# Kernel tuning notes

Hardware: AMD Instinct MI355X
Metric: run time of the kernel (lower is better)

The kernel has to match this reference:

```python
import jax, jax.numpy as jnp
import numpy as np

H = 16          # num_heads
KVH = 4         # num_kv_heads
HD = 128        # head_dim = dim // num_heads
BASE = 10000.0  # rope_base
EPS = 1.1920928955078125e-07  # torch F.rms_norm default eps = finfo(fp32).eps


def rotate_half(x):
    h = x.shape[-1] // 2
    return jnp.concatenate([-x[..., h:], x[..., :h]], axis=-1)


def rms_norm(x):
    return x * jax.lax.rsqrt(jnp.mean(x * x, axis=-1, keepdims=True) + EPS)


def setup_inputs() -> dict:
    key = jax.random.key(0)
    ks = jax.random.split(key, 5)
    D = H * HD
    KVD = KVH * HD
    s = 0.02
    x = jax.random.normal(ks[0], (4, 2048, D), jnp.float32)
    Wq = jax.random.normal(ks[1], (D, D), jnp.float32) * s
    Wk = jax.random.normal(ks[2], (KVD, D), jnp.float32) * s
    Wv = jax.random.normal(ks[3], (KVD, D), jnp.float32) * s
    Wproj = jax.random.normal(ks[4], (D, D), jnp.float32) * s
    q_gain = jnp.full((H,), 1.0, jnp.float32)
    return {"x": x, "Wq": Wq, "Wk": Wk, "Wv": Wv, "Wproj": Wproj, "q_gain": q_gain}


def reference(x, Wq, Wk, Wv, Wproj, q_gain):
    B, T, D = x.shape
    # QKV projections (bias-free), reshape to [B, heads, T, head_dim]
    q = (x @ Wq.T).reshape(B, T, H, HD).transpose(0, 2, 1, 3)
    k = (x @ Wk.T).reshape(B, T, KVH, HD).transpose(0, 2, 1, 3)
    v = (x @ Wv.T).reshape(B, T, KVH, HD).transpose(0, 2, 1, 3)
    # QK RMSNorm (no learned weight)
    q = rms_norm(q)
    k = rms_norm(k)
    # Rotary embedding tables [T, HD]
    t = jnp.arange(T, dtype=jnp.float32)
    inv_freq = 1.0 / (BASE ** (jnp.arange(0, HD, 2, dtype=jnp.float32) / HD))
    freqs = jnp.outer(t, inv_freq)
    emb = jnp.concatenate([freqs, freqs], axis=-1)
    cos, sin = jnp.cos(emb), jnp.sin(emb)
    # RoPE + per-head gain on q
    q = (q * cos + rotate_half(q) * sin) * q_gain[None, :, None, None]
    k = k * cos + rotate_half(k) * sin
    # GQA: repeat_interleave kv heads to match q heads
    groups = H // KVH
    k = jnp.repeat(k, groups, axis=1)
    v = jnp.repeat(v, groups, axis=1)
    # Causal scaled dot-product attention
    scores = jnp.einsum('bhqd,bhkd->bhqk', q, k) / np.float32(np.sqrt(HD))
    mask = jnp.tril(jnp.ones((T, T), dtype=bool))
    scores = jnp.where(mask, scores, -jnp.inf)
    attn = jax.nn.softmax(scores, axis=-1)
    y = jnp.einsum('bhqk,bhkd->bhqd', attn, v)
    y = y.transpose(0, 2, 1, 3).reshape(B, T, D)
    return y @ Wproj.T
```

## Files before the change

kernel.cpp:

```cpp
#include <hip/hip_runtime.h>
#include <math.h>


typedef float f32x4 __attribute__((ext_vector_type(4)));
typedef __bf16 bf16x8 __attribute__((ext_vector_type(8)));
typedef __bf16 bf16x4 __attribute__((ext_vector_type(4)));
typedef __bf16 bf16x2 __attribute__((ext_vector_type(2)));

__device__ __forceinline__ void load_lds16(const __bf16* g, __bf16* l) {
    __builtin_amdgcn_global_load_lds(
        (const __attribute__((address_space(1))) void*)g,
        (__attribute__((address_space(3))) void*)l, 16, 0, 0);
}

__device__ __forceinline__ unsigned pack_bf16(float lo, float hi) {
    union { bf16x2 v; unsigned u; } c;
    c.v = bf16x2{(__bf16)lo, (__bf16)hi};
    return c.u;
}

__global__ __launch_bounds__(256) void cvt_all(
    const float* __restrict__ x,  const float* __restrict__ Wq,
    const float* __restrict__ Wk, const float* __restrict__ Wv,
    const float* __restrict__ Wp, __bf16* __restrict__ dst)
{
    long long i = ((long long)blockIdx.x * 256 + threadIdx.x) * 4;
    if (i >= 27262976LL) return;
    const float* src;
    long long off;
    if (i < 16777216LL)      { src = x;  off = i; }
    else if (i < 20971520LL) { src = Wq; off = i - 16777216LL; }
    else if (i < 22020096LL) { src = Wk; off = i - 20971520LL; }
    else if (i < 23068672LL) { src = Wv; off = i - 22020096LL; }
    else                     { src = Wp; off = i - 23068672LL; }
    float4 v = *(const float4*)(src + off);
    bf16x4 o = {(__bf16)v.x, (__bf16)v.y, (__bf16)v.z, (__bf16)v.w};
    *(bf16x4*)(dst + i) = o;
}

template <typename OutT>
__global__ __launch_bounds__(512, 2) void gemm8ph(
    const __bf16* __restrict__ A, const __bf16* __restrict__ W,
    OutT* __restrict__ C, int M, int N, int K)
{
    const int bm = blockIdx.x, bn = blockIdx.y;
    const int tid = threadIdx.x;
    const int lane = tid & 63, wave = tid >> 6;
    const int quad = lane >> 4, l16 = lane & 15;
    const int wm2 = wave >> 2;
    const int wn4 = wave & 3;

    __shared__ __bf16 As[2][256 * 64];
    __shared__ __bf16 Bs[2][256 * 64];

    f32x4 acc[8][4] = {};

    const int sr = tid >> 3;
    const int sc = tid & 7;
    const int scs = sc ^ (((sr >> 2) & 1) << 1);
    const __bf16* Ag = A + (size_t)(bm * 256 + sr) * K + scs * 8;
    const __bf16* Wg = W + (size_t)(bn * 256 + sr) * K + scs * 8;
    const int dst = sr * 64 + sc * 8;

    auto stA = [&](int t, int r) {
        load_lds16(Ag + (size_t)(r * 64) * K + t * 64,
                   &As[t & 1][r * 4096 + dst]);
    };
    auto stB = [&](int t, int r) {
        load_lds16(Wg + (size_t)(r * 64) * K + t * 64,
                   &Bs[t & 1][r * 4096 + dst]);
    };

    const int NT = K / 64;
    const int swzr = ((l16 >> 2) & 1) << 1;

#pragma unroll
    for (int r = 0; r < 4; ++r) { stA(0, r); stB(0, r); }
#pragma unroll
    for (int r = 0; r < 4; ++r) { stA(1, r); stB(1, r); }
    asm volatile("s_waitcnt vmcnt(8)" ::: "memory");
    __builtin_amdgcn_s_barrier();

    bf16x8 bfr[4][2];

    for (int i = 0; i < NT / 2; ++i) {
        const int t0 = 2 * i;
#pragma unroll
        for (int tt = 0; tt < 2; ++tt) {
            const __bf16* Ab = &As[tt][0];
            const __bf16* Bb = &Bs[tt][0];
#pragma unroll
            for (int qq = 0; qq < 4; ++qq) {
                bf16x8 af[2][2];
#pragma unroll
                for (int j = 0; j < 2; ++j)
#pragma unroll
                    for (int ks = 0; ks < 2; ++ks)
                        af[j][ks] = *(const bf16x8*)(
                            Ab + (wm2 * 128 + (qq * 2 + j) * 16 + l16) * 64 +
                            ((ks * 4 + quad) ^ swzr) * 8);
                if (qq == 0) {
#pragma unroll
                    for (int ni = 0; ni < 4; ++ni)
#pragma unroll
                        for (int ks = 0; ks < 2; ++ks)
                            bfr[ni][ks] = *(const bf16x8*)(
                                Bb + (wn4 * 64 + ni * 16 + l16) * 64 +
                                ((ks * 4 + quad) ^ swzr) * 8);
                }

                const int p = tt * 4 + qq;
                switch (p) {
                    case 0: if (i > 0) { stA(t0 + 1, 1); stA(t0 + 1, 3); } break;
                    case 1: if (t0 + 2 < NT) { stB(t0 + 2, 0); stB(t0 + 2, 1); } break;
                    case 2: if (t0 + 2 < NT) { stA(t0 + 2, 0); stA(t0 + 2, 2); } break;
                    case 3: if (t0 + 2 < NT) { stB(t0 + 2, 2); stB(t0 + 2, 3); } break;
                    case 4: if (t0 + 2 < NT) { stA(t0 + 2, 1); stA(t0 + 2, 3); } break;
                    case 5: if (t0 + 3 < NT) { stB(t0 + 3, 0); stB(t0 + 3, 1); } break;
                    case 6: if (t0 + 3 < NT) { stA(t0 + 3, 0); stA(t0 + 3, 2); } break;
                    case 7: if (t0 + 3 < NT) { stB(t0 + 3, 2); stB(t0 + 3, 3); } break;
                }
                if (qq == 3)
                    asm volatile("s_waitcnt vmcnt(6)" ::: "memory");

                __builtin_amdgcn_s_barrier();
                asm volatile("s_waitcnt lgkmcnt(0)" ::: "memory");
                __builtin_amdgcn_sched_barrier(0);
                __builtin_amdgcn_s_setprio(1);
#pragma unroll
                for (int j = 0; j < 2; ++j)
#pragma unroll
                    for (int ni = 0; ni < 4; ++ni)
#pragma unroll
                        for (int ks = 0; ks < 2; ++ks)
                            acc[qq * 2 + j][ni] =
                                __builtin_amdgcn_mfma_f32_16x16x32_bf16(
                                    af[j][ks], bfr[ni][ks],
                                    acc[qq * 2 + j][ni], 0, 0, 0);
                __builtin_amdgcn_s_setprio(0);
                __builtin_amdgcn_s_barrier();
            }
        }
    }

#pragma unroll
    for (int mi = 0; mi < 8; ++mi) {
#pragma unroll
        for (int r = 0; r < 4; ++r) {
            int row = bm * 256 + wm2 * 128 + mi * 16 + quad * 4 + r;
            OutT* Cp = C + (size_t)row * N + bn * 256 + wn4 * 64 + l16;
#pragma unroll
            for (int ni = 0; ni < 4; ++ni)
                Cp[ni * 16] = (OutT)acc[mi][ni][r];
        }
    }
}

template <int NI, typename OutT>
__global__ __launch_bounds__(512, 2) void gemm4buf(
    const __bf16* __restrict__ A, const __bf16* __restrict__ W,
    OutT* __restrict__ C, int M, int N, int K)
{
    constexpr int BN = 64 * NI;
    constexpr int WN = 16 * NI;
    const int bm = blockIdx.x, bn = blockIdx.y;
    const int tid = threadIdx.x;
    const int lane = tid & 63;
    const int wave = tid >> 6;
    const int quad = lane >> 4, l16 = lane & 15;
    const int wm2 = wave >> 2;
    const int wn4 = wave & 3;

    __shared__ __bf16 As[4][256 * 32];
    __shared__ __bf16 Bs[4][BN * 32];

    f32x4 acc[8][NI] = {};

    const int sr = tid >> 2;
    const int sc = tid & 3;
    const int scs = sc ^ (sr & 3) ^ ((sr >> 2) & 3);
    const int swzq = quad ^ (l16 & 3) ^ ((l16 >> 2) & 3);

    const __bf16* Ag = A + (size_t)(bm * 256 + sr) * K + scs * 8;
    const __bf16* Wg = W + (size_t)(bn * BN + sr) * K + scs * 8;
    const int dA = sr * 32 + sc * 8;

    auto stageB = [&](int t) {
        const int k0 = t * 32, buf = t & 3;
        load_lds16(Wg + k0, &Bs[buf][dA]);
        if constexpr (NI == 4)
            load_lds16(Wg + (size_t)128 * K + k0, &Bs[buf][128 * 32 + dA]);
    };
    auto stageA = [&](int t) {
        const int k0 = t * 32, buf = t & 3;
        load_lds16(Ag + k0, &As[buf][dA]);
        load_lds16(Ag + (size_t)128 * K + k0, &As[buf][128 * 32 + dA]);
    };
    auto waitAhead = [&](int ahead) {
        if constexpr (NI == 4) {
            if (ahead >= 2)      asm volatile("s_waitcnt vmcnt(8)" ::: "memory");
            else if (ahead == 1) asm volatile("s_waitcnt vmcnt(4)" ::: "memory");
            else                 asm volatile("s_waitcnt vmcnt(0)" ::: "memory");
        } else {
            if (ahead >= 2)      asm volatile("s_waitcnt vmcnt(6)" ::: "memory");
            else if (ahead == 1) asm volatile("s_waitcnt vmcnt(3)" ::: "memory");
            else                 asm volatile("s_waitcnt vmcnt(0)" ::: "memory");
        }
    };

    const int NT = K / 32;

    stageB(0); stageA(0);
    stageB(1); stageA(1);
    stageB(2); stageA(2);
    waitAhead(2);
    asm volatile("" ::: "memory");
    __builtin_amdgcn_s_barrier();
    asm volatile("" ::: "memory");

    for (int t = 0; t < NT; ++t) {
        const __bf16* Ab = &As[t & 3][0];
        const __bf16* Bb = &Bs[t & 3][0];
        const bool pf = (t + 3 < NT);

        bf16x8 bfr[NI];
#pragma unroll
        for (int ni = 0; ni < NI; ++ni)
            bfr[ni] = *(const bf16x8*)(
                Bb + (wn4 * WN + ni * 16 + l16) * 32 + swzq * 8);
        if (pf) stageB(t + 3);

        bf16x8 af[8];
#pragma unroll
        for (int mi = 0; mi < 8; ++mi)
            af[mi] = *(const bf16x8*)(
                Ab + (wm2 * 128 + mi * 16 + l16) * 32 + swzq * 8);
        if (pf) stageA(t + 3);

        __builtin_amdgcn_s_setprio(1);
#pragma unroll
        for (int mi = 0; mi < 8; ++mi)
#pragma unroll
            for (int ni = 0; ni < NI; ++ni)
                acc[mi][ni] = __builtin_amdgcn_mfma_f32_16x16x32_bf16(
                    af[mi], bfr[ni], acc[mi][ni], 0, 0, 0);
        __builtin_amdgcn_s_setprio(0);

        if (t + 1 < NT) {
            const int hi = (t + 3 < NT - 1) ? (t + 3) : (NT - 1);
            waitAhead(hi - (t + 1));
            asm volatile("" ::: "memory");
            __builtin_amdgcn_s_barrier();
            asm volatile("" ::: "memory");
        }
    }

#pragma unroll
    for (int mi = 0; mi < 8; ++mi) {
#pragma unroll
        for (int r = 0; r < 4; ++r) {
            int row = bm * 256 + wm2 * 128 + mi * 16 + quad * 4 + r;
            OutT* Cp = C + (size_t)row * N + bn * BN + wn4 * WN + l16;
#pragma unroll
            for (int ni = 0; ni < NI; ++ni)
                Cp[ni * 16] = (OutT)acc[mi][ni][r];
        }
    }
}

__global__ __launch_bounds__(256) void k_norm_rope(__bf16* __restrict__ kv)
{
    const int row = blockIdx.x * 4 + (threadIdx.x >> 6);
    const int lane = threadIdx.x & 63;
    const int bt = row >> 2, kvh = row & 3;
    __bf16* base = kv + (size_t)bt * 1024 + kvh * 128;
    const int t = bt & 2047;

    float x0 = (float)base[lane];
    float x1 = (float)base[lane + 64];

    float ss = x0 * x0 + x1 * x1;
#pragma unroll
    for (int off = 32; off; off >>= 1) ss += __shfl_xor(ss, off);
    float inv = rsqrtf(ss * (1.0f / 128.0f) + 1.1920928955078125e-07f);
    x0 *= inv; x1 *= inv;

    float freq = exp2f(-(float)lane * 0.20762050593046013f);
    float s, c;
    __sincosf((float)t * freq, &s, &c);
    base[lane]      = (__bf16)(x0 * c - x1 * s);
    base[lane + 64] = (__bf16)(x1 * c + x0 * s);
}

__global__ __launch_bounds__(256) void transpose_v(
    const __bf16* __restrict__ kv, __bf16* __restrict__ vtout)
{
    __shared__ __bf16 tile[64][65];
    const int b = blockIdx.z;
    const int t0 = blockIdx.x * 64, c0 = blockIdx.y * 64;
    const __bf16* vb = kv + (size_t)b * 2048 * 1024 + 512;
    __bf16* vtb = vtout + (size_t)b * 512 * 2048;
    const int j = threadIdx.x & 63;
    const int r0 = threadIdx.x >> 6;
#pragma unroll
    for (int i = 0; i < 16; ++i) {
        int r = r0 + i * 4;
        tile[r][j] = vb[(size_t)(t0 + r) * 1024 + c0 + j];
    }
    __syncthreads();
#pragma unroll
    for (int i = 0; i < 16; ++i) {
        int r = r0 + i * 4;
        vtb[(size_t)(c0 + r) * 2048 + t0 + j] = tile[j][r];
    }
}

__global__ __launch_bounds__(256, 2) void attn(
    const __bf16* __restrict__ q, const __bf16* __restrict__ kv,
    const __bf16* __restrict__ vt, __bf16* __restrict__ y,
    const float* __restrict__ q_gain)
{
    const int qt = 15 - blockIdx.y;
    const int bx = blockIdx.x;
    const int g = bx & 15, j = bx >> 4;
    const int b = g >> 2, kvh = g & 3, h = kvh * 4 + j;
    const int tid = threadIdx.x;
    const int wave = tid >> 6, lane = tid & 63;
    const int quad = lane >> 4, l16 = lane & 15;

    __shared__ __bf16 Ks[2][64 * 128];
    __shared__ __bf16 Vts[2][128 * 64];
    __shared__ unsigned Ppk[2][4][16 * 32];

    const int qt0 = qt * 128;
    const int wq = wave * 16;
    const float gain = q_gain[h];

    bf16x8 qraw[2][4];
#pragma unroll
    for (int p = 0; p < 2; ++p) {
        const size_t qrow =
            ((size_t)b * 2048 + qt0 + p * 64 + wq + l16) * 2048 + h * 128;
#pragma unroll
        for (int t = 0; t < 4; ++t)
            qraw[p][t] = *(const bf16x8*)(q + qrow + t * 32 + quad * 8);
    }

    const size_t kbase = (size_t)b * 2048 * 1024 + kvh * 128;
    const size_t vtbase = (size_t)(b * 4 + kvh) * 128 * 2048;
    const int rowK = lane >> 4, pcK = lane & 15;
    const int rowV = lane >> 3, pcV = lane & 7;
    const int nj = 2 * qt + 2;

    {
#pragma unroll
        for (int r = 0; r < 4; ++r) {
            int rrK = (r * 4 + wave) * 4 + rowK;
            int cK = pcK ^ (rrK & 15);
            load_lds16(kv + kbase + (size_t)rrK * 1024 + cK * 8,
                       &Ks[0][(r * 4 + wave) * 512]);
            int rrV = (r * 4 + wave) * 8 + rowV;
            int cV = pcV ^ (rrV & 7);
            load_lds16(vt + vtbase + (size_t)rrV * 2048 + cV * 8,
                       &Vts[0][(r * 4 + wave) * 512]);
        }
    }

    bf16x8 qf[2][4];
#pragma unroll
    for (int p = 0; p < 2; ++p) {
        float xv[4][8];
        float ss = 0.f;
#pragma unroll
        for (int t = 0; t < 4; ++t)
#pragma unroll
            for (int jj = 0; jj < 8; ++jj) {
                float f = (float)qraw[p][t][jj];
                xv[t][jj] = f; ss += f * f;
            }
        ss += __shfl_xor(ss, 16);
        ss += __shfl_xor(ss, 32);
        const float sc = rsqrtf(ss * (1.0f / 128.0f) +
                                1.1920928955078125e-07f) * gain;
        const float trow = (float)(qt0 + p * 64 + wq + l16);
#pragma unroll
        for (int t = 0; t < 2; ++t)
#pragma unroll
            for (int jj = 0; jj < 8; ++jj) {
                const float fr =
                    exp2f(-(float)(t * 32 + quad * 8 + jj) * 0.20762050593046013f);
                float s, c;
                __sincosf(trow * fr, &s, &c);
                const float x0 = xv[t][jj], x1 = xv[t + 2][jj];
                qf[p][t][jj]     = (__bf16)((x0 * c - x1 * s) * sc);
                qf[p][t + 2][jj] = (__bf16)((x1 * c + x0 * s) * sc);
            }
    }

    f32x4 oacc[2][8] = {};
    float lsum[2] = {0.f, 0.f};
    const float sm_scale = 0.12754635f;
    const float mfix = 11.5f * fabsf(gain);

    for (int jt = 0; jt < nj; ++jt) {
        const int cur = jt & 1;

        asm volatile("" ::: "memory");
        __builtin_amdgcn_s_barrier();
        asm volatile("" ::: "memory");

        if (jt + 1 < nj) {
            const int j0n = (jt + 1) * 64;
#pragma unroll
            for (int r = 0; r < 4; ++r) {
                int rrK = (r * 4 + wave) * 4 + rowK;
                int cK = pcK ^ (rrK & 15);
                load_lds16(kv + kbase + (size_t)(j0n + rrK) * 1024 + cK * 8,
                           &Ks[cur ^ 1][(r * 4 + wave) * 512]);
                int rrV = (r * 4 + wave) * 8 + rowV;
                int cV = pcV ^ (rrV & 7);
                load_lds16(vt + vtbase + (size_t)rrV * 2048 + j0n + cV * 8,
                           &Vts[cur ^ 1][(r * 4 + wave) * 512]);
            }
            asm volatile("s_waitcnt vmcnt(8)" ::: "memory");
        } else {
            asm volatile("s_waitcnt vmcnt(0)" ::: "memory");
        }

        asm volatile("" ::: "memory");
        __builtin_amdgcn_s_barrier();
        asm volatile("" ::: "memory");

        const __bf16* Kc = Ks[cur];
        const __bf16* Vc = Vts[cur];

        f32x4 sacc[2][4] = {};
        __builtin_amdgcn_s_setprio(1);
#pragma unroll
        for (int nt = 0; nt < 4; ++nt)
#pragma unroll
            for (int t = 0; t < 4; ++t) {
                bf16x8 kf = *(const bf16x8*)(
                    Kc + (nt * 16 + l16) * 128 + ((t * 4 + quad) ^ l16) * 8);
                sacc[0][nt] = __builtin_amdgcn_mfma_f32_16x16x32_bf16(
                    kf, qf[0][t], sacc[0][nt], 0, 0, 0);
                sacc[1][nt] = __builtin_amdgcn_mfma_f32_16x16x32_bf16(
                    kf, qf[1][t], sacc[1][nt], 0, 0, 0);
            }
        __builtin_amdgcn_s_setprio(0);

        if (jt >= 2 * qt) {
            const int dj = jt - 2 * qt;
#pragma unroll
            for (int p = 0; p < 2; ++p) {
                const int rel = (p - dj) * 64 + wq + l16;
#pragma unroll
                for (int nt = 0; nt < 4; ++nt) {
                    const int kvb = nt * 16 + quad * 4;
#pragma unroll
                    for (int r = 0; r < 4; ++r)
                        if (kvb + r > rel) sacc[p][nt][r] = -3.0e38f;
                }
            }
        }

#pragma unroll
        for (int p = 0; p < 2; ++p) {
            unsigned* Pw = &Ppk[p][wave][0];
            const int wb = l16 * 32 + (quad & 1) * 2;
            float ls = 0.f;
#pragma unroll
            for (int nt = 0; nt < 4; ++nt) {
                float e0 = exp2f((sacc[p][nt][0] - mfix) * sm_scale);
                float e1 = exp2f((sacc[p][nt][1] - mfix) * sm_scale);
                float e2 = exp2f((sacc[p][nt][2] - mfix) * sm_scale);
                float e3 = exp2f((sacc[p][nt][3] - mfix) * sm_scale);
                ls += (e0 + e1) + (e2 + e3);
                uint2 u;
                u.x = pack_bf16(e0, e1);
                u.y = pack_bf16(e2, e3);
                *(uint2*)(Pw + wb + (((nt * 2 + (quad >> 1)) ^ (l16 & 7)) << 2)) = u;
            }
            lsum[p] += ls;
        }

        __builtin_amdgcn_s_setprio(1);
#pragma unroll
        for (int kt = 0; kt < 2; ++kt) {
            const int pcc = (kt * 4 + quad) ^ (l16 & 7);
            union { uint4 u; bf16x8 v; } c0, c1;
            c0.u = *(const uint4*)(&Ppk[0][wave][0] + l16 * 32 + (pcc << 2));
            c1.u = *(const uint4*)(&Ppk[1][wave][0] + l16 * 32 + (pcc << 2));
#pragma unroll
            for (int vn = 0; vn < 8; ++vn) {
                bf16x8 vf = *(const bf16x8*)(
                    Vc + (vn * 16 + l16) * 64 + pcc * 8);
                oacc[0][vn] = __builtin_amdgcn_mfma_f32_16x16x32_bf16(
                    vf, c0.v, oacc[0][vn], 0, 0, 0);
                oacc[1][vn] = __builtin_amdgcn_mfma_f32_16x16x32_bf16(
                    vf, c1.v, oacc[1][vn], 0, 0, 0);
            }
        }
        __builtin_amdgcn_s_setprio(0);
    }

#pragma unroll
    for (int p = 0; p < 2; ++p) {
        lsum[p] += __shfl_xor(lsum[p], 16);
        lsum[p] += __shfl_xor(lsum[p], 32);
        const float inv = 1.0f / lsum[p];
        const size_t ybase =
            ((size_t)b * 2048 + qt0 + p * 64 + wq + l16) * 2048 +
            h * 128 + quad * 4;
#pragma unroll
        for (int vn = 0; vn < 8; ++vn) {
            bf16x4 o = {(__bf16)(oacc[p][vn][0] * inv),
                        (__bf16)(oacc[p][vn][1] * inv),
                        (__bf16)(oacc[p][vn][2] * inv),
                        (__bf16)(oacc[p][vn][3] * inv)};
            *(bf16x4*)(y + ybase + vn * 16) = o;
        }
    }
}

extern "C" void kernel_launch(void* const* d_in, const int* in_sizes, int n_in,
                              void* d_out, int out_size, void* d_ws, size_t ws_size,
                              hipStream_t stream) {
    const float* x     = (const float*)d_in[0];
    const float* Wq    = (const float*)d_in[1];
    const float* Wk    = (const float*)d_in[2];
    const float* Wv    = (const float*)d_in[3];
    const float* Wproj = (const float*)d_in[4];
    const float* qgain = (const float*)d_in[5];
    float* outp = (float*)d_out;

    __bf16* xb  = (__bf16*)d_ws;
    __bf16* Wqb = xb  + 16777216;
    __bf16* Wkb = Wqb + 4194304;
    __bf16* Wvb = Wkb + 1048576;
    __bf16* Wpb = Wvb + 1048576;
    __bf16* q   = Wpb + 4194304;
    __bf16* kvb = q   + 16777216;
    __bf16* vt  = kvb + 8388608;
    __bf16* y   = q;

    dim3 blk(256);
    cvt_all<<<dim3(27262976 / 1024), blk, 0, stream>>>(x, Wq, Wk, Wv, Wproj, xb);

    gemm8ph<__bf16><<<dim3(32, 8), dim3(512), 0, stream>>>(xb, Wqb, q, 8192, 2048, 2048);
    gemm4buf<2, __bf16><<<dim3(32, 8), dim3(512), 0, stream>>>(xb, Wkb, kvb, 8192, 1024, 2048);
    k_norm_rope<<<dim3((4 * 2048 * 4) / 4), blk, 0, stream>>>(kvb);
    transpose_v<<<dim3(32, 8, 4), blk, 0, stream>>>(kvb, vt);
    attn<<<dim3(64, 16), blk, 0, stream>>>(q, kvb, vt, y, qgain);
    gemm8ph<float><<<dim3(32, 8), dim3(512), 0, stream>>>(y, Wpb, outp, 8192, 2048, 2048);
}
```

Measured before the change: 451.9 us.

## Read K and V fragments directly from global memory instead of LDS staging

Removes the double-buffered LDS staging of K and V tiles, including the async global-to-LDS loads, the waitcnt and both block barriers per iteration. Each wave now loads its K and V MFMA fragments straight from global memory, relying on L1/L2 caching. This frees LDS and removes synchronisation, but each of the four waves re-fetches the same K/V data. Load latency is also no longer hidden by prefetching.

```diff
diff --git a/kernel.cpp b/kernel.cpp
--- a/kernel.cpp
+++ b/kernel.cpp
@@ -328,8 +328,6 @@
     const int wave = tid >> 6, lane = tid & 63;
     const int quad = lane >> 4, l16 = lane & 15;
 
-    __shared__ __bf16 Ks[2][64 * 128];
-    __shared__ __bf16 Vts[2][128 * 64];
     __shared__ unsigned Ppk[2][4][16 * 32];
 
     const int qt0 = qt * 128;
@@ -348,23 +346,7 @@
 
     const size_t kbase = (size_t)b * 2048 * 1024 + kvh * 128;
     const size_t vtbase = (size_t)(b * 4 + kvh) * 128 * 2048;
-    const int rowK = lane >> 4, pcK = lane & 15;
-    const int rowV = lane >> 3, pcV = lane & 7;
     const int nj = 2 * qt + 2;
-
-    {
-#pragma unroll
-        for (int r = 0; r < 4; ++r) {
-            int rrK = (r * 4 + wave) * 4 + rowK;
-            int cK = pcK ^ (rrK & 15);
-            load_lds16(kv + kbase + (size_t)rrK * 1024 + cK * 8,
-                       &Ks[0][(r * 4 + wave) * 512]);
-            int rrV = (r * 4 + wave) * 8 + rowV;
-            int cV = pcV ^ (rrV & 7);
-            load_lds16(vt + vtbase + (size_t)rrV * 2048 + cV * 8,
-                       &Vts[0][(r * 4 + wave) * 512]);
-        }
-    }
 
     bf16x8 qf[2][4];
 #pragma unroll
@@ -403,50 +385,22 @@
     const float mfix = 11.5f * fabsf(gain);
 
     for (int jt = 0; jt < nj; ++jt) {
-        const int cur = jt & 1;
-
-        asm volatile("" ::: "memory");
-        __builtin_amdgcn_s_barrier();
-        asm volatile("" ::: "memory");
-
-        if (jt + 1 < nj) {
-            const int j0n = (jt + 1) * 64;
-#pragma unroll
-            for (int r = 0; r < 4; ++r) {
-                int rrK = (r * 4 + wave) * 4 + rowK;
-                int cK = pcK ^ (rrK & 15);
-                load_lds16(kv + kbase + (size_t)(j0n + rrK) * 1024 + cK * 8,
-                           &Ks[cur ^ 1][(r * 4 + wave) * 512]);
-                int rrV = (r * 4 + wave) * 8 + rowV;
-                int cV = pcV ^ (rrV & 7);
-                load_lds16(vt + vtbase + (size_t)rrV * 2048 + j0n + cV * 8,
-                           &Vts[cur ^ 1][(r * 4 + wave) * 512]);
-            }
-            asm volatile("s_waitcnt vmcnt(8)" ::: "memory");
-        } else {
-            asm volatile("s_waitcnt vmcnt(0)" ::: "memory");
-        }
-
-        asm volatile("" ::: "memory");
-        __builtin_amdgcn_s_barrier();
-        asm volatile("" ::: "memory");
-
-        const __bf16* Kc = Ks[cur];
-        const __bf16* Vc = Vts[cur];
+        const int j0 = jt * 64;
 
         f32x4 sacc[2][4] = {};
         __builtin_amdgcn_s_setprio(1);
 #pragma unroll
-        for (int nt = 0; nt < 4; ++nt)
+        for (int nt = 0; nt < 4; ++nt) {
+            const __bf16* Krow = kv + kbase + (size_t)(j0 + nt * 16 + l16) * 1024;
 #pragma unroll
             for (int t = 0; t < 4; ++t) {
-                bf16x8 kf = *(const bf16x8*)(
-                    Kc + (nt * 16 + l16) * 128 + ((t * 4 + quad) ^ l16) * 8);
+                bf16x8 kf = *(const bf16x8*)(Krow + (t * 4 + quad) * 8);
                 sacc[0][nt] = __builtin_amdgcn_mfma_f32_16x16x32_bf16(
                     kf, qf[0][t], sacc[0][nt], 0, 0, 0);
                 sacc[1][nt] = __builtin_amdgcn_mfma_f32_16x16x32_bf16(
                     kf, qf[1][t], sacc[1][nt], 0, 0, 0);
             }
+        }
         __builtin_amdgcn_s_setprio(0);
 
         if (jt >= 2 * qt) {
@@ -494,7 +448,8 @@
 #pragma unroll
             for (int vn = 0; vn < 8; ++vn) {
                 bf16x8 vf = *(const bf16x8*)(
-                    Vc + (vn * 16 + l16) * 64 + pcc * 8);
+                    vt + vtbase + (size_t)(vn * 16 + l16) * 2048 + j0 +
+                    (kt * 4 + quad) * 8);
                 oacc[0][vn] = __builtin_amdgcn_mfma_f32_16x16x32_bf16(
                     vf, c0.v, oacc[0][vn], 0, 0, 0);
                 oacc[1][vn] = __builtin_amdgcn_mfma_f32_16x16x32_bf16(
```

Result: slower. 606.5 us (+34.2%).
